# Kernel tuning notes

Hardware: AMD Instinct MI355X
Metric: run time of the kernel (lower is better)

The kernel has to match this reference:

```python
import jax, jax.numpy as jnp
import numpy as np

B, QL, T, H = 32, 1, 2048, 512


def setup_inputs() -> dict:
    key = jax.random.key(0)
    ks = jax.random.split(key, 10)
    n = lambda i, shape, sc=1.0: jax.random.normal(ks[i], shape, dtype=jnp.float32) * sc
    inv = 1.0 / np.sqrt(H)
    return {
        "query": n(0, (B, QL, H)),
        "value": n(1, (B, T, H)),
        "last_attn": jax.random.uniform(ks[2], (B, T), dtype=jnp.float32),
        "conv_w": n(3, (H, 1, 3), 0.1),   # Conv1d weight (out_ch, in_ch=1, k=3)
        "conv_b": n(4, (H,), 0.1),
        "q_w": n(5, (H, H), inv),          # query_proj (no bias)
        "v_w": n(6, (H, H), inv),          # value_proj (no bias)
        "s_w": n(7, (1, H), inv),          # score_proj weight
        "s_b": n(8, (1,), 0.1),            # score_proj bias
        "bias": n(9, (H,), 0.1),           # learned additive bias
    }


def reference(query, value, last_attn, conv_w, conv_b, q_w, v_w, s_w, s_b, bias):
    Tlen = last_attn.shape[1]
    # Conv1d(in=1, out=H, k=3, pad=1) over last_attn, then transpose -> (B, T, H)
    pad = jnp.pad(last_attn, ((0, 0), (1, 1)))
    frames = jnp.stack([pad[:, k:k + Tlen] for k in range(3)], axis=0)  # (3, B, T)
    conv_attn = jnp.einsum('hk,kbt->bth', conv_w[:, 0, :], frames) + conv_b  # (B, T, H)
    q = jnp.einsum('bqh,oh->bqo', query, q_w)   # (B, 1, H)
    v = jnp.einsum('bth,oh->bto', value, v_w)   # (B, T, H)
    e = jnp.tanh(q + v + conv_attn + bias)      # (B, T, H), q broadcasts over T
    score = jnp.einsum('bth,oh->bt', e, s_w) + s_b  # (B, T)
    # smoothing=True branch: sigmoid then L1-normalize
    score = jax.nn.sigmoid(score)
    attn = score / jnp.sum(score, axis=-1, keepdims=True)
    context = jnp.einsum('bt,bth->bh', attn, value)  # bmm(attn[:,None,:], value).squeeze(1)
    return context, attn
```

## Files before the change

### kernel.cpp

```cpp
#include <hip/hip_runtime.h>
#include <math.h>

#define B 32
#define T 2048
#define H 512

#define BMT 128
#define APAD 40

typedef __attribute__((ext_vector_type(8))) __bf16 bf16x8;
typedef __attribute__((ext_vector_type(4))) __bf16 bf16x4v;
typedef __attribute__((ext_vector_type(4))) float f32x4;
typedef __attribute__((ext_vector_type(8))) float f32x8;
typedef __attribute__((ext_vector_type(4))) float floatx4;

union pack8 { bf16x4v h; uint2 u; };

static __device__ __forceinline__ float fast_tanh(float x) {
    float ex = __expf(2.f * x);
    return 1.f - 2.f * __builtin_amdgcn_rcpf(ex + 1.f);
}

__global__ __launch_bounds__(256) void k1_init(const float* __restrict__ query,
                                               const float* __restrict__ q_w,
                                               const float* __restrict__ bias,
                                               const float* __restrict__ v_w,
                                               float* __restrict__ qpb,
                                               unsigned short* __restrict__ wbf,
                                               float* __restrict__ ctx_out) {
    const int b = blockIdx.x;
    const int s = blockIdx.y;
    const int tid = threadIdx.x;

    if (s == 8) {
        const size_t base = (size_t)b * 8192 + tid * 4;
#pragma unroll
        for (int i = 0; i < 8; ++i) {
            const size_t off = base + (size_t)i * 1024;
            f32x4 a = *(const f32x4*)(v_w + off);
            pack8 p;
            p.h = __builtin_convertvector(a, bf16x4v);
            *(uint2*)(wbf + off) = p.u;
        }
        return;
    }

    const int wave = tid >> 6;
    const int lane = tid & 63;

    if (s < 2) ctx_out[b * H + s * 256 + tid] = 0.f;

    const float* qb = query + (size_t)b * H + lane * 8;
    float4 q0 = *(const float4*)qb;
    float4 q1 = *(const float4*)(qb + 4);

    const int o0 = s * 64 + wave * 16;
#pragma unroll
    for (int i = 0; i < 16; ++i) {
        const int o = o0 + i;
        const float* wr = q_w + (size_t)o * H + lane * 8;
        float4 w0 = *(const float4*)wr;
        float4 w1 = *(const float4*)(wr + 4);
        float acc = w0.x * q0.x + w0.y * q0.y + w0.z * q0.z + w0.w * q0.w +
                    w1.x * q1.x + w1.y * q1.y + w1.z * q1.z + w1.w * q1.w;
#pragma unroll
        for (int m = 1; m < 64; m <<= 1) acc += __shfl_xor(acc, m);
        if (lane == 0) qpb[b * H + o] = acc + bias[o];
    }
}

__global__ __launch_bounds__(1024, 4) void k2_big(const float* __restrict__ value,
                                                  const unsigned short* __restrict__ wbf,
                                                  const float* __restrict__ la,
                                                  const float* __restrict__ conv_w,
                                                  const float* __restrict__ conv_b,
                                                  const float* __restrict__ s_w,
                                                  const float* __restrict__ qpb,
                                                  float* __restrict__ pre) {
    __shared__ __align__(16) unsigned short As[BMT * APAD];
    __shared__ __align__(16) unsigned short Bs[H * APAD];
    __shared__ float qpbs[H], sws[H], cbs[H], cw0s[H], cw1s[H], cw2s[H];
    __shared__ float las[BMT + 2];
    __shared__ float redp[BMT][8];

    const int t0 = blockIdx.x * BMT;
    const int b  = blockIdx.y;
    const int tid = threadIdx.x;
    const int wave = tid >> 6;
    const int lane = tid & 63;
    const int tx   = lane & 15;
    const int quad = lane >> 4;
    const int wm   = (wave & 1) * 64;
    const int wn   = (wave >> 1) * 64;

    if (tid < H) {
        qpbs[tid] = qpb[b * H + tid];
        sws[tid]  = s_w[tid];
        cbs[tid]  = conv_b[tid];
        cw0s[tid] = conv_w[tid * 3 + 0];
        cw1s[tid] = conv_w[tid * 3 + 1];
        cw2s[tid] = conv_w[tid * 3 + 2];
    }
    if (tid < BMT + 2) {
        const int t = t0 + tid - 1;
        las[tid] = (t >= 0 && t < T) ? la[b * T + t] : 0.f;
    }

    floatx4 acc[4][4];
#pragma unroll
    for (int i = 0; i < 4; ++i)
#pragma unroll
        for (int j = 0; j < 4; ++j) acc[i][j] = (floatx4){0.f, 0.f, 0.f, 0.f};

    const int arow = tid >> 3;
    const int acol = (tid & 7) * 4;
    const float* agp = value + ((size_t)b * T + t0 + arow) * H + acol;
    const int brow = tid >> 1;
    const int bcol = (tid & 1) * 16;
    const unsigned short* bgp = wbf + (size_t)brow * H + bcol;

    for (int kc = 0; kc < H; kc += 32) {
        f32x4 av = *(const f32x4*)(agp + kc);
        uint4 bv0 = *(const uint4*)(bgp + kc);
        uint4 bv1 = *(const uint4*)(bgp + kc + 8);

        __syncthreads();

        pack8 p;
        p.h = __builtin_convertvector(av, bf16x4v);
        *(uint2*)&As[arow * APAD + acol] = p.u;
        *(uint4*)&Bs[brow * APAD + bcol] = bv0;
        *(uint4*)&Bs[brow * APAD + bcol + 8] = bv1;

        __syncthreads();

        bf16x8 af[4], bfr[4];
#pragma unroll
        for (int mi = 0; mi < 4; ++mi)
            af[mi] = *(const bf16x8*)&As[(wm + mi * 16 + tx) * APAD + quad * 8];
#pragma unroll
        for (int ni = 0; ni < 4; ++ni)
            bfr[ni] = *(const bf16x8*)&Bs[(wn + ni * 16 + tx) * APAD + quad * 8];
#pragma unroll
        for (int mi = 0; mi < 4; ++mi)
#pragma unroll
            for (int ni = 0; ni < 4; ++ni)
                acc[mi][ni] = __builtin_amdgcn_mfma_f32_16x16x32_bf16(
                    af[mi], bfr[ni], acc[mi][ni], 0, 0, 0);
    }

    float sacc[16];
#pragma unroll
    for (int i = 0; i < 16; ++i) sacc[i] = 0.f;

#pragma unroll
    for (int ni = 0; ni < 4; ++ni) {
        const int ol = wn + ni * 16 + tx;
        const float c0 = cw0s[ol], c1 = cw1s[ol], c2 = cw2s[ol];
        const float cb = cbs[ol], qp = qpbs[ol], sw = sws[ol];
#pragma unroll
        for (int mi = 0; mi < 4; ++mi)
#pragma unroll
            for (int r = 0; r < 4; ++r) {
                const int tl = wm + mi * 16 + quad * 4 + r;
                const float conv = c0 * las[tl] + c1 * las[tl + 1] + c2 * las[tl + 2] + cb;
                const float x = acc[mi][ni][r] + qp + conv;
                sacc[mi * 4 + r] += sw * fast_tanh(x);
            }
    }
    __syncthreads();
#pragma unroll
    for (int i = 0; i < 16; ++i) {
        float v = sacc[i];
        v += __shfl_xor(v, 1);
        v += __shfl_xor(v, 2);
        v += __shfl_xor(v, 4);
        v += __shfl_xor(v, 8);
        if (tx == 0) {
            const int tl = wm + (i >> 2) * 16 + quad * 4 + (i & 3);
            redp[tl][wave >> 1] = v;
        }
    }
    __syncthreads();
    if (tid < BMT) {
        float p = 0.f;
#pragma unroll
        for (int w = 0; w < 8; ++w) p += redp[tid][w];
        pre[b * T + t0 + tid] = p;
    }
}

__global__ __launch_bounds__(256) void k3_fused(const float* __restrict__ value,
                                                const float* __restrict__ pre,
                                                const float* __restrict__ s_b,
                                                float* __restrict__ attn_out,
                                                float* __restrict__ ctx) {
    __shared__ float sm[T];
    __shared__ float red[4];
    __shared__ float redc[4][H];
    const int b = blockIdx.x;
    const int slice = blockIdx.y;
    const int tid = threadIdx.x;
    const float sb = s_b[0];

    float s[8];
    float loc = 0.f;
#pragma unroll
    for (int i = 0; i < 8; ++i) {
        const int t = tid + i * 256;
        const float p = pre[b * T + t] + sb;
        const float sg = 1.f / (1.f + expf(-p));
        s[i] = sg;
        sm[t] = sg;
        loc += sg;
    }
#pragma unroll
    for (int m = 1; m < 64; m <<= 1) loc += __shfl_xor(loc, m);
    if ((tid & 63) == 0) red[tid >> 6] = loc;
    __syncthreads();
    const float inv = 1.f / (red[0] + red[1] + red[2] + red[3]);
    if (slice == 0) {
#pragma unroll
        for (int i = 0; i < 8; ++i) attn_out[b * T + tid + i * 256] = s[i] * inv;
    }

    const int col = (tid & 63) * 8;
    const int tp  = tid >> 6;
    f32x8 a;
#pragma unroll
    for (int i = 0; i < 8; ++i) a[i] = 0.f;
    const float* vb = value + (size_t)b * T * H + col;
    const int tbeg = slice * 128;
    for (int t = tbeg + tp; t < tbeg + 128; t += 4) {
        const float w = sm[t] * inv;
        f32x4 v0 = *(const f32x4*)(vb + (size_t)t * H);
        f32x4 v1 = *(const f32x4*)(vb + (size_t)t * H + 4);
#pragma unroll
        for (int i = 0; i < 4; ++i) { a[i] += w * v0[i]; a[i + 4] += w * v1[i]; }
    }
    *(f32x4*)&redc[tp][col]     = (f32x4){a[0], a[1], a[2], a[3]};
    *(f32x4*)&redc[tp][col + 4] = (f32x4){a[4], a[5], a[6], a[7]};
    __syncthreads();
    if (tid < 128) {
        const int h = tid * 4;
        f32x4 r0 = *(const f32x4*)&redc[0][h];
        f32x4 r1 = *(const f32x4*)&redc[1][h];
        f32x4 r2 = *(const f32x4*)&redc[2][h];
        f32x4 r3 = *(const f32x4*)&redc[3][h];
        atomicAdd(&ctx[b * H + h + 0], r0[0] + r1[0] + r2[0] + r3[0]);
        atomicAdd(&ctx[b * H + h + 1], r0[1] + r1[1] + r2[1] + r3[1]);
        atomicAdd(&ctx[b * H + h + 2], r0[2] + r1[2] + r2[2] + r3[2]);
        atomicAdd(&ctx[b * H + h + 3], r0[3] + r1[3] + r2[3] + r3[3]);
    }
}

extern "C" void kernel_launch(void* const* d_in, const int* in_sizes, int n_in,
                              void* d_out, int out_size, void* d_ws, size_t ws_size,
                              hipStream_t stream) {
    const float* query  = (const float*)d_in[0];
    const float* value  = (const float*)d_in[1];
    const float* la     = (const float*)d_in[2];
    const float* conv_w = (const float*)d_in[3];
    const float* conv_b = (const float*)d_in[4];
    const float* q_w    = (const float*)d_in[5];
    const float* v_w    = (const float*)d_in[6];
    const float* s_w    = (const float*)d_in[7];
    const float* s_b    = (const float*)d_in[8];
    const float* bias   = (const float*)d_in[9];

    float* out  = (float*)d_out;
    float* ctx  = out;
    float* attn = out + B * H;

    float* qpb = (float*)d_ws;
    float* pre = qpb + B * H;
    unsigned short* wbf = (unsigned short*)(pre + B * T);

    dim3 g1(B, 9);
    k1_init<<<g1, 256, 0, stream>>>(query, q_w, bias, v_w, qpb, wbf, ctx);

    dim3 g2(T / BMT, B);
    k2_big<<<g2, 1024, 0, stream>>>(value, wbf, la, conv_w, conv_b, s_w, qpb, pre);

    dim3 g3(B, 16);
    k3_fused<<<g3, 256, 0, stream>>>(value, pre, s_b, attn, ctx);
}
```

Measured before the change: 306.0 us.

## Fuse context accumulation into score GEMM kernel with deferred normalization

The score GEMM kernel now applies the sigmoid itself and accumulates unnormalized context (sigmoid-weighted value rows) plus a per-batch denominator through atomics, reusing its own value tile. A small final kernel divides both attn and context by the denominator. This removes the second full pass over value that the old third kernel made. The GEMM tile also shrinks to 64 rows with 512 threads, and the bf16 weight tile is loaded with direct global-to-LDS loads. In exchange there are more atomics and more blocks, and the LDS weight layout is unpadded, which may cause bank conflicts.

New measurement: 280.3 us. 1.09x faster.

```diff
diff --git a/kernel.cpp b/kernel.cpp
--- a/kernel.cpp
+++ b/kernel.cpp
@@ -5,35 +5,45 @@
 #define T 2048
 #define H 512
 
-#define BMT 128
+#define BT2 64
 #define APAD 40
 
 typedef __attribute__((ext_vector_type(8))) __bf16 bf16x8;
 typedef __attribute__((ext_vector_type(4))) __bf16 bf16x4v;
 typedef __attribute__((ext_vector_type(4))) float f32x4;
-typedef __attribute__((ext_vector_type(8))) float f32x8;
 typedef __attribute__((ext_vector_type(4))) float floatx4;
 
 union pack8 { bf16x4v h; uint2 u; };
 
-static __device__ __forceinline__ float fast_tanh(float x) {
-    float ex = __expf(2.f * x);
-    return 1.f - 2.f * __builtin_amdgcn_rcpf(ex + 1.f);
-}
-
-__global__ __launch_bounds__(256) void k1_init(const float* __restrict__ query,
-                                               const float* __restrict__ q_w,
-                                               const float* __restrict__ bias,
-                                               const float* __restrict__ v_w,
-                                               float* __restrict__ qpb,
-                                               unsigned short* __restrict__ wbf,
-                                               float* __restrict__ ctx_out) {
-    const int b = blockIdx.x;
-    const int s = blockIdx.y;
+static __device__ __forceinline__ void gl_lds16(const void* g, void* l) {
+    __builtin_amdgcn_global_load_lds(
+        (const __attribute__((address_space(1))) void*)g,
+        (__attribute__((address_space(3))) void*)l, 16, 0, 0);
+}
+
+__global__ __launch_bounds__(256) void k_init(const float* __restrict__ query,
+                                              const float* __restrict__ q_w,
+                                              const float* __restrict__ bias,
+                                              const float* __restrict__ v_w,
+                                              float* __restrict__ qpb,
+                                              unsigned short* __restrict__ wbf,
+                                              float* __restrict__ ctx_num,
+                                              float* __restrict__ denom) {
+    const int blk = blockIdx.x;
     const int tid = threadIdx.x;
 
-    if (s == 8) {
-        const size_t base = (size_t)b * 8192 + tid * 4;
+    if (blk >= 288) {
+#pragma unroll
+        for (int i = 0; i < 16; ++i) {
+            const int off = tid * 4 + i * 1024;
+            *(f32x4*)(ctx_num + off) = (f32x4){0.f, 0.f, 0.f, 0.f};
+        }
+        if (tid < B) denom[tid] = 0.f;
+        return;
+    }
+    if (blk >= 256) {
+        const int c = blk - 256;
+        const size_t base = (size_t)c * 8192 + tid * 4;
 #pragma unroll
         for (int i = 0; i < 8; ++i) {
             const size_t off = base + (size_t)i * 1024;
@@ -45,10 +55,10 @@
         return;
     }
 
+    const int b = blk >> 3;
+    const int s = blk & 7;
     const int wave = tid >> 6;
     const int lane = tid & 63;
-
-    if (s < 2) ctx_out[b * H + s * 256 + tid] = 0.f;
 
     const float* qb = query + (size_t)b * H + lane * 8;
     float4 q0 = *(const float4*)qb;
@@ -69,41 +79,47 @@
     }
 }
 
-__global__ __launch_bounds__(1024, 4) void k2_big(const float* __restrict__ value,
-                                                  const unsigned short* __restrict__ wbf,
-                                                  const float* __restrict__ la,
-                                                  const float* __restrict__ conv_w,
-                                                  const float* __restrict__ conv_b,
-                                                  const float* __restrict__ s_w,
-                                                  const float* __restrict__ qpb,
-                                                  float* __restrict__ pre) {
-    __shared__ __align__(16) unsigned short As[BMT * APAD];
-    __shared__ __align__(16) unsigned short Bs[H * APAD];
-    __shared__ float qpbs[H], sws[H], cbs[H], cw0s[H], cw1s[H], cw2s[H];
-    __shared__ float las[BMT + 2];
-    __shared__ float redp[BMT][8];
-
-    const int t0 = blockIdx.x * BMT;
+__global__ __launch_bounds__(512, 4) void k2_fused(const float* __restrict__ value,
+                                                   const unsigned short* __restrict__ wbf,
+                                                   const float* __restrict__ la,
+                                                   const float* __restrict__ conv_w,
+                                                   const float* __restrict__ conv_b,
+                                                   const float* __restrict__ s_w,
+                                                   const float* __restrict__ qpb,
+                                                   const float* __restrict__ s_b,
+                                                   float* __restrict__ pre_sg,
+                                                   float* __restrict__ ctx_num,
+                                                   float* __restrict__ denom) {
+    __shared__ __align__(16) unsigned short As[BT2 * APAD];
+    __shared__ __align__(16) unsigned short Bs[H * 32];
+    __shared__ float las[BT2 + 2];
+    __shared__ float redp[BT2][9];
+    __shared__ float sgs[BT2];
+
+    const int t0 = blockIdx.x * BT2;
     const int b  = blockIdx.y;
     const int tid = threadIdx.x;
     const int wave = tid >> 6;
     const int lane = tid & 63;
     const int tx   = lane & 15;
     const int quad = lane >> 4;
-    const int wm   = (wave & 1) * 64;
-    const int wn   = (wave >> 1) * 64;
-
-    if (tid < H) {
-        qpbs[tid] = qpb[b * H + tid];
-        sws[tid]  = s_w[tid];
-        cbs[tid]  = conv_b[tid];
-        cw0s[tid] = conv_w[tid * 3 + 0];
-        cw1s[tid] = conv_w[tid * 3 + 1];
-        cw2s[tid] = conv_w[tid * 3 + 2];
-    }
-    if (tid < BMT + 2) {
+    const int wn   = wave * 64;
+
+    if (tid < BT2 + 2) {
         const int t = t0 + tid - 1;
         las[tid] = (t >= 0 && t < T) ? la[b * T + t] : 0.f;
+    }
+
+    float qp4[4], sw4[4], cb4[4], c04[4], c14[4], c24[4];
+#pragma unroll
+    for (int ni = 0; ni < 4; ++ni) {
+        const int ol = wn + ni * 16 + tx;
+        qp4[ni] = qpb[b * H + ol];
+        sw4[ni] = s_w[ol];
+        cb4[ni] = conv_b[ol];
+        c04[ni] = conv_w[ol * 3 + 0];
+        c14[ni] = conv_w[ol * 3 + 1];
+        c24[ni] = conv_w[ol * 3 + 2];
     }
 
     floatx4 acc[4][4];
@@ -115,32 +131,37 @@
     const int arow = tid >> 3;
     const int acol = (tid & 7) * 4;
     const float* agp = value + ((size_t)b * T + t0 + arow) * H + acol;
-    const int brow = tid >> 1;
-    const int bcol = (tid & 1) * 16;
-    const unsigned short* bgp = wbf + (size_t)brow * H + bcol;
+    const int brow = lane >> 2;
+    const int bcol = (lane & 3) * 8;
+    const unsigned short* gB[4];
+    unsigned short* lB[4];
+#pragma unroll
+    for (int c = 0; c < 4; ++c) {
+        const int chunk = wave + c * 8;
+        gB[c] = wbf + (size_t)(chunk * 16 + brow) * H + bcol;
+        lB[c] = &Bs[chunk * 512];
+    }
 
     for (int kc = 0; kc < H; kc += 32) {
         f32x4 av = *(const f32x4*)(agp + kc);
-        uint4 bv0 = *(const uint4*)(bgp + kc);
-        uint4 bv1 = *(const uint4*)(bgp + kc + 8);
 
         __syncthreads();
+#pragma unroll
+        for (int c = 0; c < 4; ++c) gl_lds16(gB[c] + kc, lB[c]);
 
         pack8 p;
         p.h = __builtin_convertvector(av, bf16x4v);
         *(uint2*)&As[arow * APAD + acol] = p.u;
-        *(uint4*)&Bs[brow * APAD + bcol] = bv0;
-        *(uint4*)&Bs[brow * APAD + bcol + 8] = bv1;
 
         __syncthreads();
 
         bf16x8 af[4], bfr[4];
 #pragma unroll
         for (int mi = 0; mi < 4; ++mi)
-            af[mi] = *(const bf16x8*)&As[(wm + mi * 16 + tx) * APAD + quad * 8];
+            af[mi] = *(const bf16x8*)&As[(mi * 16 + tx) * APAD + quad * 8];
 #pragma unroll
         for (int ni = 0; ni < 4; ++ni)
-            bfr[ni] = *(const bf16x8*)&Bs[(wn + ni * 16 + tx) * APAD + quad * 8];
+            bfr[ni] = *(const bf16x8*)&Bs[(wn + ni * 16 + tx) * 32 + quad * 8];
 #pragma unroll
         for (int mi = 0; mi < 4; ++mi)
 #pragma unroll
@@ -152,23 +173,21 @@
     float sacc[16];
 #pragma unroll
     for (int i = 0; i < 16; ++i) sacc[i] = 0.f;
-
 #pragma unroll
     for (int ni = 0; ni < 4; ++ni) {
-        const int ol = wn + ni * 16 + tx;
-        const float c0 = cw0s[ol], c1 = cw1s[ol], c2 = cw2s[ol];
-        const float cb = cbs[ol], qp = qpbs[ol], sw = sws[ol];
 #pragma unroll
         for (int mi = 0; mi < 4; ++mi)
 #pragma unroll
             for (int r = 0; r < 4; ++r) {
-                const int tl = wm + mi * 16 + quad * 4 + r;
-                const float conv = c0 * las[tl] + c1 * las[tl + 1] + c2 * las[tl + 2] + cb;
-                const float x = acc[mi][ni][r] + qp + conv;
-                sacc[mi * 4 + r] += sw * fast_tanh(x);
+                const int tl = mi * 16 + quad * 4 + r;
+                const float conv = c04[ni] * las[tl] + c14[ni] * las[tl + 1] +
+                                   c24[ni] * las[tl + 2] + cb4[ni];
+                const float x = acc[mi][ni][r] + qp4[ni] + conv;
+                const float ex = __expf(2.f * x);
+                const float th = 1.f - 2.f * __builtin_amdgcn_rcpf(ex + 1.f);
+                sacc[mi * 4 + r] += sw4[ni] * th;
             }
     }
-    __syncthreads();
 #pragma unroll
     for (int i = 0; i < 16; ++i) {
         float v = sacc[i];
@@ -176,81 +195,66 @@
         v += __shfl_xor(v, 2);
         v += __shfl_xor(v, 4);
         v += __shfl_xor(v, 8);
-        if (tx == 0) {
-            const int tl = wm + (i >> 2) * 16 + quad * 4 + (i & 3);
-            redp[tl][wave >> 1] = v;
-        }
+        if (tx == 0) redp[(i >> 2) * 16 + quad * 4 + (i & 3)][wave] = v;
     }
     __syncthreads();
-    if (tid < BMT) {
-        float p = 0.f;
-#pragma unroll
-        for (int w = 0; w < 8; ++w) p += redp[tid][w];
-        pre[b * T + t0 + tid] = p;
-    }
-}
-
-__global__ __launch_bounds__(256) void k3_fused(const float* __restrict__ value,
-                                                const float* __restrict__ pre,
-                                                const float* __restrict__ s_b,
-                                                float* __restrict__ attn_out,
-                                                float* __restrict__ ctx) {
-    __shared__ float sm[T];
-    __shared__ float red[4];
-    __shared__ float redc[4][H];
-    const int b = blockIdx.x;
-    const int slice = blockIdx.y;
-    const int tid = threadIdx.x;
-    const float sb = s_b[0];
-
-    float s[8];
-    float loc = 0.f;
-#pragma unroll
-    for (int i = 0; i < 8; ++i) {
-        const int t = tid + i * 256;
-        const float p = pre[b * T + t] + sb;
-        const float sg = 1.f / (1.f + expf(-p));
-        s[i] = sg;
-        sm[t] = sg;
-        loc += sg;
-    }
-#pragma unroll
-    for (int m = 1; m < 64; m <<= 1) loc += __shfl_xor(loc, m);
-    if ((tid & 63) == 0) red[tid >> 6] = loc;
+
+    if (tid < BT2) {
+        float sc = s_b[0];
+#pragma unroll
+        for (int w = 0; w < 8; ++w) sc += redp[tid][w];
+        const float sg = 1.f / (1.f + __expf(-sc));
+        sgs[tid] = sg;
+        pre_sg[b * T + t0 + tid] = sg;
+        float dsum = sg;
+#pragma unroll
+        for (int m = 1; m < 64; m <<= 1) dsum += __shfl_xor(dsum, m);
+        if (tid == 0) atomicAdd(&denom[b], dsum);
+    }
     __syncthreads();
-    const float inv = 1.f / (red[0] + red[1] + red[2] + red[3]);
-    if (slice == 0) {
-#pragma unroll
-        for (int i = 0; i < 8; ++i) attn_out[b * T + tid + i * 256] = s[i] * inv;
-    }
-
-    const int col = (tid & 63) * 8;
-    const int tp  = tid >> 6;
-    f32x8 a;
-#pragma unroll
-    for (int i = 0; i < 8; ++i) a[i] = 0.f;
-    const float* vb = value + (size_t)b * T * H + col;
-    const int tbeg = slice * 128;
-    for (int t = tbeg + tp; t < tbeg + 128; t += 4) {
-        const float w = sm[t] * inv;
-        f32x4 v0 = *(const f32x4*)(vb + (size_t)t * H);
-        f32x4 v1 = *(const f32x4*)(vb + (size_t)t * H + 4);
-#pragma unroll
-        for (int i = 0; i < 4; ++i) { a[i] += w * v0[i]; a[i + 4] += w * v1[i]; }
-    }
-    *(f32x4*)&redc[tp][col]     = (f32x4){a[0], a[1], a[2], a[3]};
-    *(f32x4*)&redc[tp][col + 4] = (f32x4){a[4], a[5], a[6], a[7]};
+
+    float* redc = (float*)Bs;
+    const int h4 = (tid & 127) * 4;
+    const int tp = tid >> 7;
+    f32x4 a = {0.f, 0.f, 0.f, 0.f};
+    const float* vb = value + ((size_t)b * T + t0) * H + h4;
+    for (int t = tp; t < BT2; t += 4) {
+        const float w = sgs[t];
+        f32x4 v = *(const f32x4*)(vb + (size_t)t * H);
+        a.x += w * v.x; a.y += w * v.y; a.z += w * v.z; a.w += w * v.w;
+    }
+    *(f32x4*)&redc[tp * 512 + h4] = a;
     __syncthreads();
     if (tid < 128) {
         const int h = tid * 4;
-        f32x4 r0 = *(const f32x4*)&redc[0][h];
-        f32x4 r1 = *(const f32x4*)&redc[1][h];
-        f32x4 r2 = *(const f32x4*)&redc[2][h];
-        f32x4 r3 = *(const f32x4*)&redc[3][h];
-        atomicAdd(&ctx[b * H + h + 0], r0[0] + r1[0] + r2[0] + r3[0]);
-        atomicAdd(&ctx[b * H + h + 1], r0[1] + r1[1] + r2[1] + r3[1]);
-        atomicAdd(&ctx[b * H + h + 2], r0[2] + r1[2] + r2[2] + r3[2]);
-        atomicAdd(&ctx[b * H + h + 3], r0[3] + r1[3] + r2[3] + r3[3]);
+        f32x4 r0 = *(const f32x4*)&redc[0 * 512 + h];
+        f32x4 r1 = *(const f32x4*)&redc[1 * 512 + h];
+        f32x4 r2 = *(const f32x4*)&redc[2 * 512 + h];
+        f32x4 r3 = *(const f32x4*)&redc[3 * 512 + h];
+        atomicAdd(&ctx_num[b * H + h + 0], r0.x + r1.x + r2.x + r3.x);
+        atomicAdd(&ctx_num[b * H + h + 1], r0.y + r1.y + r2.y + r3.y);
+        atomicAdd(&ctx_num[b * H + h + 2], r0.z + r1.z + r2.z + r3.z);
+        atomicAdd(&ctx_num[b * H + h + 3], r0.w + r1.w + r2.w + r3.w);
+    }
+}
+
+__global__ __launch_bounds__(256) void k3_scale(const float* __restrict__ pre_sg,
+                                                const float* __restrict__ ctx_num,
+                                                const float* __restrict__ denom,
+                                                float* __restrict__ attn_out,
+                                                float* __restrict__ ctx) {
+    const int b = blockIdx.x;
+    const int tid = threadIdx.x;
+    const float inv = 1.f / denom[b];
+#pragma unroll
+    for (int i = 0; i < 8; ++i) {
+        const int t = tid + i * 256;
+        attn_out[b * T + t] = pre_sg[b * T + t] * inv;
+    }
+#pragma unroll
+    for (int i = 0; i < 2; ++i) {
+        const int h = tid + i * 256;
+        ctx[b * H + h] = ctx_num[b * H + h] * inv;
     }
 }
 
@@ -272,16 +276,17 @@
     float* ctx  = out;
     float* attn = out + B * H;
 
-    float* qpb = (float*)d_ws;
-    float* pre = qpb + B * H;
-    unsigned short* wbf = (unsigned short*)(pre + B * T);
-
-    dim3 g1(B, 9);
-    k1_init<<<g1, 256, 0, stream>>>(query, q_w, bias, v_w, qpb, wbf, ctx);
-
-    dim3 g2(T / BMT, B);
-    k2_big<<<g2, 1024, 0, stream>>>(value, wbf, la, conv_w, conv_b, s_w, qpb, pre);
-
-    dim3 g3(B, 16);
-    k3_fused<<<g3, 256, 0, stream>>>(value, pre, s_b, attn, ctx);
-}
+    float* qpb     = (float*)d_ws;
+    float* pre_sg  = qpb + B * H;
+    float* ctx_num = pre_sg + B * T;
+    float* denom   = ctx_num + B * H;
+    unsigned short* wbf = (unsigned short*)(denom + 64);
+
+    k_init<<<289, 256, 0, stream>>>(query, q_w, bias, v_w, qpb, wbf, ctx_num, denom);
+
+    dim3 g2(T / BT2, B);
+    k2_fused<<<g2, 512, 0, stream>>>(value, wbf, la, conv_w, conv_b, s_w, qpb, s_b,
+                                     pre_sg, ctx_num, denom);
+
+    k3_scale<<<B, 256, 0, stream>>>(pre_sg, ctx_num, denom, attn, ctx);
+}
```
